# Performance work log

Measured on AMD Instinct MI355X. Metric: run time of the kernel, lower is better.

Reference implementation:

```python
import jax, jax.numpy as jnp
import numpy as np

BN_EPS = 1e-5


def setup_inputs() -> dict:
    key = jax.random.key(0)
    ks = jax.random.split(key, 6)
    B, C, N = 8, 256, 4096
    C4 = C // 4
    return {
        "x": jax.random.normal(ks[0], (B, C, N), dtype=jnp.float32),
        "w_qk": jax.random.normal(ks[1], (C4, C), dtype=jnp.float32) * 0.05,  # shared q/k weight
        "w_v": jax.random.normal(ks[2], (C, C), dtype=jnp.float32) * 0.05,
        "b_v": jax.random.normal(ks[3], (C,), dtype=jnp.float32) * 0.05,
        "w_t": jax.random.normal(ks[4], (C, C), dtype=jnp.float32) * 0.05,
        "b_t": jax.random.normal(ks[5], (C,), dtype=jnp.float32) * 0.05,
        "gamma": jnp.ones((C,), dtype=jnp.float32),
        "beta": jnp.zeros((C,), dtype=jnp.float32),
        "run_mean": jnp.zeros((C,), dtype=jnp.float32),
        "run_var": jnp.ones((C,), dtype=jnp.float32),
    }


def reference(x, w_qk, w_v, b_v, w_t, b_t, gamma, beta, run_mean, run_var):
    # x: [B, C, N]; 1x1 Conv1d == channel matmul.
    x_q = jnp.einsum('oc,bcn->bno', w_qk, x)               # [B, N, C/4]
    x_k = jnp.einsum('oc,bcn->bon', w_qk, x)               # [B, C/4, N]
    energy = jnp.einsum('bno,bom->bnm', x_q, x_k)          # [B, N, N], NO 1/sqrt(d) scaling
    attn = jax.nn.softmax(energy, axis=-1)                 # softmax over last dim only
    x_v = jnp.einsum('oc,bcn->bon', w_v, x) + b_v[None, :, None]  # [B, C, N]
    x_r = jnp.einsum('bcn,bnm->bcm', x_v, attn)            # V @ attn (right-multiply, no transpose)
    t = jnp.einsum('oc,bcn->bon', w_t, x - x_r) + b_t[None, :, None]
    # BatchNorm1d (inference): per-channel affine with running stats
    inv = gamma / jnp.sqrt(run_var + BN_EPS)
    bn = t * inv[None, :, None] + (beta - run_mean * inv)[None, :, None]
    return x + jnp.maximum(bn, 0.0)
```

## Files before the change

kernel.cpp:

```cpp
#include <hip/hip_runtime.h>

#define Bb 8
#define Cc 256
#define C4 64
#define Nn 4096

typedef _Float16 half8 __attribute__((ext_vector_type(8)));
typedef float f32x4 __attribute__((ext_vector_type(4)));
typedef unsigned int u32;

__device__ __forceinline__ f32x4 fz4() {
  f32x4 z; z[0] = 0.f; z[1] = 0.f; z[2] = 0.f; z[3] = 0.f; return z;
}
__device__ __forceinline__ f32x4 mfma16(half8 a, half8 b, f32x4 c) {
  return __builtin_amdgcn_mfma_f32_16x16x32_f16(a, b, c, 0, 0, 0);
}
__device__ __forceinline__ u32 pkrtz(float a, float b) {
  typedef __fp16 h2n __attribute__((ext_vector_type(2)));
  h2n h = __builtin_amdgcn_cvt_pkrtz(a, b);
  return __builtin_bit_cast(u32, h);
}
__device__ __forceinline__ void gll16(const void* g, void* l) {
  __builtin_amdgcn_global_load_lds(
      (const __attribute__((address_space(1))) u32*)g,
      (__attribute__((address_space(3))) u32*)l, 16, 0, 0);
}


__global__ void k0_weights(const float* __restrict__ wqk, const float* __restrict__ wv,
                           const float* __restrict__ wt,
                           _Float16* __restrict__ wqkh, _Float16* __restrict__ wqkl,
                           _Float16* __restrict__ wvf, _Float16* __restrict__ wtf) {
  int idx = blockIdx.x * 256 + threadIdx.x;
  if (idx < C4 * Cc) {
    int o = idx >> 8, c = idx & 255;
    float f = wqk[idx] * 1.2011224087864498f;
    _Float16 h = (_Float16)f;
    int off = ((((o >> 4) * 8 + (c >> 5)) * 4 + ((c >> 3) & 3)) * 16 + (o & 15)) * 8 + (c & 7);
    wqkh[off] = h;
    wqkl[off] = (_Float16)(f - (float)h);
  }
  if (idx < Cc * Cc) {
    int o = idx >> 8, k = idx & 255;
    int off = ((((o >> 4) * 8 + (k >> 5)) * 4 + ((k >> 3) & 3)) * 16 + (o & 15)) * 8 + (k & 7);
    wvf[off] = (_Float16)wv[idx];
    wtf[off] = (_Float16)wt[idx];
  }
}

__global__ __launch_bounds__(512) void k23_qkv(
    const float* __restrict__ x,
    const _Float16* __restrict__ wqkh, const _Float16* __restrict__ wqkl,
    const _Float16* __restrict__ wvf, const float* __restrict__ bv,
    _Float16* __restrict__ qkf, _Float16* __restrict__ xvf) {
  __shared__ _Float16 xh[64 * 264];
  const int bid = blockIdx.x;
  const int b = bid & 7, n0 = (bid >> 3) * 64, tid = threadIdx.x;
  {
    const int cc = tid >> 3, nn = (tid & 7) * 8;
    #pragma unroll
    for (int ph = 0; ph < 4; ++ph) {
      int c = cc + ph * 64;
      const float* src = x + ((size_t)(b * Cc + c)) * Nn + n0 + nn;
      float4 v0 = *(const float4*)(src);
      float4 v1 = *(const float4*)(src + 4);
      float vv[8] = {v0.x, v0.y, v0.z, v0.w, v1.x, v1.y, v1.z, v1.w};
      #pragma unroll
      for (int j = 0; j < 8; ++j) xh[(nn + j) * 264 + c] = (_Float16)vv[j];
    }
  }
  __syncthreads();
  const int w = tid >> 6, lane = tid & 63, l15 = lane & 15, l4 = lane >> 4;
  {
    const int fn = w >> 1, ob = (w & 1) * 32;
    f32x4 acc[2] = {fz4(), fz4()};
    #pragma unroll
    for (int kb = 0; kb < 8; ++kb) {
      half8 ah = *(const half8*)(xh + (fn * 16 + l15) * 264 + kb * 32 + l4 * 8);
      #pragma unroll
      for (int f = 0; f < 2; ++f) {
        const int ot = (ob >> 4) + f;
        half8 bh = *(const half8*)((const char*)wqkh + (ot * 8 + kb) * 1024 + lane * 16);
        half8 bl = *(const half8*)((const char*)wqkl + (ot * 8 + kb) * 1024 + lane * 16);
        acc[f] = mfma16(ah, bh, acc[f]);
        acc[f] = mfma16(ah, bl, acc[f]);
      }
    }
    #pragma unroll
    for (int f = 0; f < 2; ++f)
      #pragma unroll
      for (int i = 0; i < 4; ++i) {
        const int n = n0 + fn * 16 + l4 * 4 + i;
        const int o = ob + f * 16 + l15;
        int off = ((((b * 256 + (n >> 4)) * 2 + (o >> 5)) * 4 + ((o >> 3) & 3)) * 16 +
                   (n & 15)) * 8 + (o & 7);
        qkf[off] = (_Float16)acc[f][i];
      }
  }
  {
    const int cb = w * 32;
    f32x4 acc[2][4];
    #pragma unroll
    for (int a = 0; a < 2; ++a)
      #pragma unroll
      for (int q = 0; q < 4; ++q) acc[a][q] = fz4();
    #pragma unroll
    for (int kb = 0; kb < 8; ++kb) {
      half8 bfr[4];
      #pragma unroll
      for (int fnb = 0; fnb < 4; ++fnb)
        bfr[fnb] = *(const half8*)(xh + (fnb * 16 + l15) * 264 + kb * 32 + l4 * 8);
      #pragma unroll
      for (int fc = 0; fc < 2; ++fc) {
        const int ct = (cb >> 4) + fc;
        half8 a = *(const half8*)((const char*)wvf + (ct * 8 + kb) * 1024 + lane * 16);
        #pragma unroll
        for (int fnb = 0; fnb < 4; ++fnb)
          acc[fc][fnb] = mfma16(a, bfr[fnb], acc[fc][fnb]);
      }
    }
    #pragma unroll
    for (int fc = 0; fc < 2; ++fc)
      #pragma unroll
      for (int fnb = 0; fnb < 4; ++fnb)
        #pragma unroll
        for (int i = 0; i < 4; ++i) {
          const int c = cb + fc * 16 + l4 * 4 + i;
          const int n = n0 + fnb * 16 + l15;
          int off = ((((b * 16 + (c >> 4)) * 128 + (n >> 5)) * 4 + ((n >> 3) & 3)) * 16 +
                     (c & 15)) * 8 + (n & 7);
          xvf[off] = (_Float16)(acc[fc][fnb][i] + bv[c]);
        }
  }
}

__global__ __launch_bounds__(512, 4) void k4_stats(
    const _Float16* __restrict__ qkf, float* __restrict__ stats) {
  __shared__ float red[64][8];
  const int bid = blockIdx.x;
  const int b = bid & 7, n0 = (bid >> 3) * 64, tid = threadIdx.x;
  const int w = tid >> 6, lane = tid & 63, l15 = lane & 15, l4 = lane >> 4;
  const char* qbt = (const char*)qkf + (size_t)b * 524288;

  half8 qn_r[2][4];
  #pragma unroll
  for (int kb = 0; kb < 2; ++kb)
    #pragma unroll
    for (int fn = 0; fn < 4; ++fn)
      qn_r[kb][fn] = *(const half8*)(qbt + (((n0 >> 4) + fn) * 2 + kb) * 1024 + lane * 16);

  const char* qp = qbt + w * 2048 + lane * 16;
  half8 qa0 = *(const half8*)qp;
  half8 qa1 = *(const half8*)(qp + 1024);

  float sm[4] = {0.f, 0.f, 0.f, 0.f};
  for (int it = 0; it < 32; ++it) {
    f32x4 g[4] = {fz4(), fz4(), fz4(), fz4()};
    #pragma unroll
    for (int fn = 0; fn < 4; ++fn) g[fn] = mfma16(qa0, qn_r[0][fn], g[fn]);
    #pragma unroll
    for (int fn = 0; fn < 4; ++fn) g[fn] = mfma16(qa1, qn_r[1][fn], g[fn]);
    if (it < 31) qp += 16384;
    qa0 = *(const half8*)qp;
    qa1 = *(const half8*)(qp + 1024);
    #pragma unroll
    for (int fn = 0; fn < 4; ++fn)
      #pragma unroll
      for (int i = 0; i < 4; ++i)
        sm[fn] += exp2f(g[fn][i] - 32.0f);
  }
  #pragma unroll
  for (int fn = 0; fn < 4; ++fn) {
    sm[fn] += __shfl_xor(sm[fn], 16, 64);
    sm[fn] += __shfl_xor(sm[fn], 32, 64);
  }
  if (l4 == 0) {
    #pragma unroll
    for (int fn = 0; fn < 4; ++fn) red[fn * 16 + l15][w] = sm[fn];
  }
  __syncthreads();
  if (tid < 64) {
    float t = 0.f;
    #pragma unroll
    for (int j = 0; j < 8; ++j) t += red[tid][j];
    stats[(size_t)b * Nn + n0 + tid] = 32.0f + log2f(t);
  }
}

__global__ __launch_bounds__(512, 4) void k5_main(
    const float* __restrict__ x,
    const _Float16* __restrict__ qkf, const _Float16* __restrict__ xvf,
    const float* __restrict__ stats,
    const _Float16* __restrict__ wtf, const float* __restrict__ bt,
    const float* __restrict__ gamma, const float* __restrict__ beta,
    const float* __restrict__ rmean, const float* __restrict__ rvar,
    float* __restrict__ out) {
  __shared__ __align__(16) char smem[73728];
  const int bid = blockIdx.x;
  const int b = bid & 7, m0 = (bid >> 3) * 64, tid = threadIdx.x;
  const int w = tid >> 6, lane = tid & 63, l15 = lane & 15, l4 = lane >> 4;
  const int wa = w >> 2;
  const int wb = w & 3;
  const size_t bq = (size_t)b * Nn;
  const char* qkt = (const char*)qkf + (size_t)b * 524288;
  const char* xvt = (const char*)xvf + (size_t)b * 2097152;
  const int key = l15 & 7;
  char* xvw = smem + 40960 + (w << 12);

  half8 qm_r[2][2];
  #pragma unroll
  for (int kb = 0; kb < 2; ++kb)
    #pragma unroll
    for (int fm = 0; fm < 2; ++fm)
      qm_r[kb][fm] = *(const half8*)(qkt + (((m0 >> 4) + wa * 2 + fm) * 2 + kb) * 1024 +
                                     lane * 16);

  const char* qnsrc = qkt + 16384 + (size_t)tid * 16;
  const char* xvsrc[4];
  #pragma unroll
  for (int j = 0; j < 4; ++j)
    xvsrc[j] = xvt + ((w * 2 + (j >> 1)) * 128 + (j & 1)) * 1024 + (size_t)lane * 16;
  const float* anp = stats + bq + wb * 16 + l4 * 4;

  f32x4 acc[4][2];
  #pragma unroll
  for (int a = 0; a < 4; ++a)
    #pragma unroll
    for (int q = 0; q < 2; ++q) acc[a][q] = fz4();

  gll16(qkt + (size_t)tid * 16, smem + w * 1024);
  gll16(qkt + 8192 + (size_t)tid * 16, smem + 8192 + w * 1024);
  #pragma unroll
  for (int j = 0; j < 4; ++j) gll16(xvsrc[j], xvw + j * 1024);
  float4 an = *(const float4*)anp;
  asm volatile("s_waitcnt vmcnt(0) lgkmcnt(0)" ::: "memory");
  __builtin_amdgcn_sched_barrier(0);
  __builtin_amdgcn_s_barrier();

  int br = 0, bw = 2;
  for (int it = 0; it < 64; ++it) {
    gll16(qnsrc, smem + bw * 8192 + w * 1024);
    if (it < 61) qnsrc += 8192;
    bw = bw == 2 ? 0 : bw + 1;
    const char* qb = smem + br * 8192;
    br = br == 2 ? 0 : br + 1;
    f32x4 g0 = fz4(), g1 = fz4();
    #pragma unroll
    for (int kb = 0; kb < 2; ++kb) {
      half8 ah = *(const half8*)(qb + wb * 2048 + kb * 1024 + lane * 16);
      g0 = mfma16(ah, qm_r[kb][0], g0);
      g1 = mfma16(ah, qm_r[kb][1], g1);
    }
    char* PTp = smem + 24576 + ((it & 1) << 13);
    {
      uint2 pk;
      pk.x = pkrtz(exp2f(g0[0] - an.x), exp2f(g0[1] - an.y));
      pk.y = pkrtz(exp2f(g0[2] - an.z), exp2f(g0[3] - an.w));
      *(uint2*)(PTp + (wa * 32 + l15) * 128 + ((wb * 32 + l4 * 8) ^ (key << 4))) = pk;
      pk.x = pkrtz(exp2f(g1[0] - an.x), exp2f(g1[1] - an.y));
      pk.y = pkrtz(exp2f(g1[2] - an.z), exp2f(g1[3] - an.w));
      *(uint2*)(PTp + (wa * 32 + 16 + l15) * 128 + ((wb * 32 + l4 * 8) ^ (key << 4))) = pk;
    }
    if (it < 63) anp += 64;
    an = *(const float4*)anp;
    asm volatile("s_waitcnt vmcnt(2) lgkmcnt(0)" ::: "memory");
    __builtin_amdgcn_sched_barrier(0);
    __builtin_amdgcn_s_barrier();
    __builtin_amdgcn_s_setprio(1);
    #pragma unroll
    for (int kb = 0; kb < 2; ++kb) {
      half8 pa[4], xb[2];
      #pragma unroll
      for (int fm = 0; fm < 4; ++fm)
        pa[fm] = *(const half8*)(PTp + (fm * 16 + l15) * 128 + (((kb * 4 + l4) ^ key) * 16));
      #pragma unroll
      for (int fc = 0; fc < 2; ++fc)
        xb[fc] = *(const half8*)(xvw + (fc * 2 + kb) * 1024 + lane * 16);
      #pragma unroll
      for (int fm = 0; fm < 4; ++fm)
        #pragma unroll
        for (int fc = 0; fc < 2; ++fc)
          acc[fm][fc] = mfma16(pa[fm], xb[fc], acc[fm][fc]);
    }
    __builtin_amdgcn_s_setprio(0);
    asm volatile("s_waitcnt lgkmcnt(0)" ::: "memory");
    __builtin_amdgcn_sched_barrier(0);
    if (it < 63) {
      #pragma unroll
      for (int j = 0; j < 4; ++j) xvsrc[j] += 2048;
    }
    #pragma unroll
    for (int j = 0; j < 4; ++j) gll16(xvsrc[j], xvw + j * 1024);
  }
  asm volatile("s_waitcnt vmcnt(0) lgkmcnt(0)" ::: "memory");
  __builtin_amdgcn_sched_barrier(0);
  __builtin_amdgcn_s_barrier();

  _Float16* st = (_Float16*)smem;
  #pragma unroll
  for (int fm = 0; fm < 4; ++fm)
    #pragma unroll
    for (int fc = 0; fc < 2; ++fc) {
      int c = w * 32 + fc * 16 + l15;
      const float* xp = x + ((size_t)b * Cc + c) * Nn + m0 + fm * 16 + l4 * 4;
      float4 v = *(const float4*)xp;
      float vv[4] = {v.x, v.y, v.z, v.w};
      #pragma unroll
      for (int i = 0; i < 4; ++i) {
        int m = fm * 16 + l4 * 4 + i;
        st[m * 264 + c] = (_Float16)(vv[i] - acc[fm][fc][i]);
      }
    }
  __syncthreads();
  {
    const int ob = (w >> 1) * 64, mb2 = (w & 1) * 32;
    f32x4 t[4][2];
    #pragma unroll
    for (int a = 0; a < 4; ++a)
      #pragma unroll
      for (int q = 0; q < 2; ++q) t[a][q] = fz4();
    #pragma unroll
    for (int kb = 0; kb < 8; ++kb) {
      half8 bfr[2];
      #pragma unroll
      for (int fm2 = 0; fm2 < 2; ++fm2)
        bfr[fm2] = *(const half8*)(st + (mb2 + fm2 * 16 + l15) * 264 + kb * 32 + l4 * 8);
      #pragma unroll
      for (int fo = 0; fo < 4; ++fo) {
        const int ot = (ob >> 4) + fo;
        half8 a = *(const half8*)((const char*)wtf + (ot * 8 + kb) * 1024 + lane * 16);
        #pragma unroll
        for (int fm2 = 0; fm2 < 2; ++fm2)
          t[fo][fm2] = mfma16(a, bfr[fm2], t[fo][fm2]);
      }
    }
    #pragma unroll
    for (int fo = 0; fo < 4; ++fo)
      #pragma unroll
      for (int i = 0; i < 4; ++i) {
        const int o = ob + fo * 16 + l4 * 4 + i;
        const float inv = gamma[o] * rsqrtf(rvar[o] + 1e-5f);
        const float addv = beta[o] - rmean[o] * inv;
        const float btv = bt[o];
        #pragma unroll
        for (int fm2 = 0; fm2 < 2; ++fm2) {
          const int m = m0 + mb2 + fm2 * 16 + l15;
          float tv = t[fo][fm2][i] + btv;
          float bn = tv * inv + addv;
          float xr = x[((size_t)b * Cc + o) * Nn + m];
          out[((size_t)b * Cc + o) * Nn + m] = xr + fmaxf(bn, 0.0f);
        }
      }
  }
}

extern "C" void kernel_launch(void* const* d_in, const int* in_sizes, int n_in,
                              void* d_out, int out_size, void* d_ws, size_t ws_size,
                              hipStream_t stream) {
  const float* x = (const float*)d_in[0];
  const float* wqk = (const float*)d_in[1];
  const float* wv = (const float*)d_in[2];
  const float* bv = (const float*)d_in[3];
  const float* wt = (const float*)d_in[4];
  const float* bt = (const float*)d_in[5];
  const float* gamma = (const float*)d_in[6];
  const float* beta = (const float*)d_in[7];
  const float* rmean = (const float*)d_in[8];
  const float* rvar = (const float*)d_in[9];
  float* out = (float*)d_out;

  char* ws = (char*)d_ws;
  size_t off = 0;
  auto alloc = [&](size_t nb) {
    char* p = ws + off;
    off += (nb + 255) & ~(size_t)255;
    return p;
  };
  _Float16* qkf = (_Float16*)alloc((size_t)Bb * Nn * C4 * 2);
  _Float16* xvf = (_Float16*)alloc((size_t)Bb * Cc * Nn * 2);
  float* stats = (float*)alloc((size_t)Bb * Nn * 4);
  _Float16* wqkh = (_Float16*)alloc((size_t)C4 * Cc * 2);
  _Float16* wqkl = (_Float16*)alloc((size_t)C4 * Cc * 2);
  _Float16* wvf = (_Float16*)alloc((size_t)Cc * Cc * 2);
  _Float16* wtf = (_Float16*)alloc((size_t)Cc * Cc * 2);

  k0_weights<<<dim3(256), dim3(256), 0, stream>>>(wqk, wv, wt, wqkh, wqkl, wvf, wtf);
  k23_qkv<<<dim3(512), dim3(512), 0, stream>>>(x, wqkh, wqkl, wvf, bv, qkf, xvf);
  k4_stats<<<dim3(512), dim3(512), 0, stream>>>(qkf, stats);
  k5_main<<<dim3(512), dim3(512), 0, stream>>>(x, qkf, xvf, stats, wtf, bt,
                                               gamma, beta, rmean, rvar, out);
}
```

Baseline: 164.9 us.

## Double output tile per block in attention kernel and use raw v_exp_f32

The main attention kernel now handles 128 output columns per block instead of 64. Its 8 waves are laid out as a 2x4 grid, each computing a 64x64 accumulator tile, and the xv tiles are double-buffered in a shared LDS region. This halves the grid to 256 blocks and doubles reuse of each streamed V tile and each softmax probability tile. The cost is more LDS (120KB) and more registers, with launch bounds lowered to 2 blocks per CU. exp2f is also replaced with a raw v_exp_f32 instruction to avoid range-handling overhead, at the risk of losing denormal or edge-case accuracy.

```diff
diff --git a/kernel.cpp b/kernel.cpp
--- a/kernel.cpp
+++ b/kernel.cpp
@@ -19,6 +19,11 @@
   typedef __fp16 h2n __attribute__((ext_vector_type(2)));
   h2n h = __builtin_amdgcn_cvt_pkrtz(a, b);
   return __builtin_bit_cast(u32, h);
+}
+__device__ __forceinline__ float ex2(float x) {
+  float r;
+  asm("v_exp_f32 %0, %1" : "=v"(r) : "v"(x));
+  return r;
 }
 __device__ __forceinline__ void gll16(const void* g, void* l) {
   __builtin_amdgcn_global_load_lds(
@@ -167,7 +172,7 @@
     for (int fn = 0; fn < 4; ++fn)
       #pragma unroll
       for (int i = 0; i < 4; ++i)
-        sm[fn] += exp2f(g[fn][i] - 32.0f);
+        sm[fn] += ex2(g[fn][i] - 32.0f);
   }
   #pragma unroll
   for (int fn = 0; fn < 4; ++fn) {
@@ -187,7 +192,7 @@
   }
 }
 
-__global__ __launch_bounds__(512, 4) void k5_main(
+__global__ __launch_bounds__(512, 2) void k5_main(
     const float* __restrict__ x,
     const _Float16* __restrict__ qkf, const _Float16* __restrict__ xvf,
     const float* __restrict__ stats,
@@ -195,9 +200,9 @@
     const float* __restrict__ gamma, const float* __restrict__ beta,
     const float* __restrict__ rmean, const float* __restrict__ rvar,
     float* __restrict__ out) {
-  __shared__ __align__(16) char smem[73728];
+  __shared__ __align__(16) char smem[122880];
   const int bid = blockIdx.x;
-  const int b = bid & 7, m0 = (bid >> 3) * 64, tid = threadIdx.x;
+  const int b = bid & 7, m0 = (bid >> 3) * 128, tid = threadIdx.x;
   const int w = tid >> 6, lane = tid & 63, l15 = lane & 15, l4 = lane >> 4;
   const int wa = w >> 2;
   const int wb = w & 3;
@@ -205,33 +210,30 @@
   const char* qkt = (const char*)qkf + (size_t)b * 524288;
   const char* xvt = (const char*)xvf + (size_t)b * 2097152;
   const int key = l15 & 7;
-  char* xvw = smem + 40960 + (w << 12);
-
-  half8 qm_r[2][2];
+
+  half8 qm_r[2][4];
   #pragma unroll
   for (int kb = 0; kb < 2; ++kb)
     #pragma unroll
-    for (int fm = 0; fm < 2; ++fm)
-      qm_r[kb][fm] = *(const half8*)(qkt + (((m0 >> 4) + wa * 2 + fm) * 2 + kb) * 1024 +
+    for (int fm = 0; fm < 4; ++fm)
+      qm_r[kb][fm] = *(const half8*)(qkt + ((((m0 >> 4) + wa * 4 + fm) * 2) + kb) * 1024 +
                                      lane * 16);
 
   const char* qnsrc = qkt + 16384 + (size_t)tid * 16;
-  const char* xvsrc[4];
-  #pragma unroll
-  for (int j = 0; j < 4; ++j)
-    xvsrc[j] = xvt + ((w * 2 + (j >> 1)) * 128 + (j & 1)) * 1024 + (size_t)lane * 16;
+  const char* xvp = xvt + (size_t)w * 262144 + (size_t)lane * 16;
   const float* anp = stats + bq + wb * 16 + l4 * 4;
 
-  f32x4 acc[4][2];
+  f32x4 acc[4][4];
   #pragma unroll
   for (int a = 0; a < 4; ++a)
     #pragma unroll
-    for (int q = 0; q < 2; ++q) acc[a][q] = fz4();
+    for (int q = 0; q < 4; ++q) acc[a][q] = fz4();
 
   gll16(qkt + (size_t)tid * 16, smem + w * 1024);
   gll16(qkt + 8192 + (size_t)tid * 16, smem + 8192 + w * 1024);
   #pragma unroll
-  for (int j = 0; j < 4; ++j) gll16(xvsrc[j], xvw + j * 1024);
+  for (int j = 0; j < 4; ++j)
+    gll16(xvp + (j >> 1) * 131072 + (j & 1) * 1024, smem + 57344 + (w * 4 + j) * 1024);
   float4 an = *(const float4*)anp;
   asm volatile("s_waitcnt vmcnt(0) lgkmcnt(0)" ::: "memory");
   __builtin_amdgcn_sched_barrier(0);
@@ -244,53 +246,52 @@
     bw = bw == 2 ? 0 : bw + 1;
     const char* qb = smem + br * 8192;
     br = br == 2 ? 0 : br + 1;
-    f32x4 g0 = fz4(), g1 = fz4();
+    f32x4 g[4] = {fz4(), fz4(), fz4(), fz4()};
     #pragma unroll
     for (int kb = 0; kb < 2; ++kb) {
-      half8 ah = *(const half8*)(qb + wb * 2048 + kb * 1024 + lane * 16);
-      g0 = mfma16(ah, qm_r[kb][0], g0);
-      g1 = mfma16(ah, qm_r[kb][1], g1);
-    }
-    char* PTp = smem + 24576 + ((it & 1) << 13);
-    {
+      half8 ah = *(const half8*)(qb + (wb * 2 + kb) * 1024 + lane * 16);
+      #pragma unroll
+      for (int fm = 0; fm < 4; ++fm)
+        g[fm] = mfma16(ah, qm_r[kb][fm], g[fm]);
+    }
+    char* PTp = smem + 24576 + ((it & 1) << 14);
+    #pragma unroll
+    for (int fm = 0; fm < 4; ++fm) {
       uint2 pk;
-      pk.x = pkrtz(exp2f(g0[0] - an.x), exp2f(g0[1] - an.y));
-      pk.y = pkrtz(exp2f(g0[2] - an.z), exp2f(g0[3] - an.w));
-      *(uint2*)(PTp + (wa * 32 + l15) * 128 + ((wb * 32 + l4 * 8) ^ (key << 4))) = pk;
-      pk.x = pkrtz(exp2f(g1[0] - an.x), exp2f(g1[1] - an.y));
-      pk.y = pkrtz(exp2f(g1[2] - an.z), exp2f(g1[3] - an.w));
-      *(uint2*)(PTp + (wa * 32 + 16 + l15) * 128 + ((wb * 32 + l4 * 8) ^ (key << 4))) = pk;
+      pk.x = pkrtz(ex2(g[fm][0] - an.x), ex2(g[fm][1] - an.y));
+      pk.y = pkrtz(ex2(g[fm][2] - an.z), ex2(g[fm][3] - an.w));
+      *(uint2*)(PTp + (wa * 64 + fm * 16 + l15) * 128 +
+                ((wb * 32 + l4 * 8) ^ (key << 4))) = pk;
     }
     if (it < 63) anp += 64;
     an = *(const float4*)anp;
     asm volatile("s_waitcnt vmcnt(2) lgkmcnt(0)" ::: "memory");
     __builtin_amdgcn_sched_barrier(0);
     __builtin_amdgcn_s_barrier();
+    const char* xvR = smem + 57344 + ((it & 1) << 15);
     __builtin_amdgcn_s_setprio(1);
     #pragma unroll
     for (int kb = 0; kb < 2; ++kb) {
-      half8 pa[4], xb[2];
+      half8 pa[4], xb[4];
       #pragma unroll
       for (int fm = 0; fm < 4; ++fm)
-        pa[fm] = *(const half8*)(PTp + (fm * 16 + l15) * 128 + (((kb * 4 + l4) ^ key) * 16));
-      #pragma unroll
-      for (int fc = 0; fc < 2; ++fc)
-        xb[fc] = *(const half8*)(xvw + (fc * 2 + kb) * 1024 + lane * 16);
+        pa[fm] = *(const half8*)(PTp + (wa * 64 + fm * 16 + l15) * 128 +
+                                 (((kb * 4 + l4) ^ key) * 16));
+      #pragma unroll
+      for (int fc = 0; fc < 4; ++fc)
+        xb[fc] = *(const half8*)(xvR + ((wb * 4 + fc) * 2 + kb) * 1024 + lane * 16);
       #pragma unroll
       for (int fm = 0; fm < 4; ++fm)
         #pragma unroll
-        for (int fc = 0; fc < 2; ++fc)
+        for (int fc = 0; fc < 4; ++fc)
           acc[fm][fc] = mfma16(pa[fm], xb[fc], acc[fm][fc]);
     }
     __builtin_amdgcn_s_setprio(0);
-    asm volatile("s_waitcnt lgkmcnt(0)" ::: "memory");
-    __builtin_amdgcn_sched_barrier(0);
-    if (it < 63) {
-      #pragma unroll
-      for (int j = 0; j < 4; ++j) xvsrc[j] += 2048;
-    }
-    #pragma unroll
-    for (int j = 0; j < 4; ++j) gll16(xvsrc[j], xvw + j * 1024);
+    if (it < 63) xvp += 2048;
+    char* xvD = smem + 57344 + (((it + 1) & 1) << 15) + (w * 4) * 1024;
+    #pragma unroll
+    for (int j = 0; j < 4; ++j)
+      gll16(xvp + (j >> 1) * 131072 + (j & 1) * 1024, xvD + j * 1024);
   }
   asm volatile("s_waitcnt vmcnt(0) lgkmcnt(0)" ::: "memory");
   __builtin_amdgcn_sched_barrier(0);
@@ -300,37 +301,36 @@
   #pragma unroll
   for (int fm = 0; fm < 4; ++fm)
     #pragma unroll
-    for (int fc = 0; fc < 2; ++fc) {
-      int c = w * 32 + fc * 16 + l15;
-      const float* xp = x + ((size_t)b * Cc + c) * Nn + m0 + fm * 16 + l4 * 4;
+    for (int fc = 0; fc < 4; ++fc) {
+      int c = wb * 64 + fc * 16 + l15;
+      int mb = wa * 64 + fm * 16 + l4 * 4;
+      const float* xp = x + ((size_t)b * Cc + c) * Nn + m0 + mb;
       float4 v = *(const float4*)xp;
       float vv[4] = {v.x, v.y, v.z, v.w};
       #pragma unroll
-      for (int i = 0; i < 4; ++i) {
-        int m = fm * 16 + l4 * 4 + i;
-        st[m * 264 + c] = (_Float16)(vv[i] - acc[fm][fc][i]);
-      }
+      for (int i = 0; i < 4; ++i)
+        st[(mb + i) * 264 + c] = (_Float16)(vv[i] - acc[fm][fc][i]);
     }
   __syncthreads();
   {
-    const int ob = (w >> 1) * 64, mb2 = (w & 1) * 32;
-    f32x4 t[4][2];
+    const int ob = wb * 64, mh = wa * 64;
+    f32x4 t[4][4];
     #pragma unroll
     for (int a = 0; a < 4; ++a)
       #pragma unroll
-      for (int q = 0; q < 2; ++q) t[a][q] = fz4();
+      for (int q = 0; q < 4; ++q) t[a][q] = fz4();
     #pragma unroll
     for (int kb = 0; kb < 8; ++kb) {
-      half8 bfr[2];
-      #pragma unroll
-      for (int fm2 = 0; fm2 < 2; ++fm2)
-        bfr[fm2] = *(const half8*)(st + (mb2 + fm2 * 16 + l15) * 264 + kb * 32 + l4 * 8);
+      half8 bfr[4];
+      #pragma unroll
+      for (int fm2 = 0; fm2 < 4; ++fm2)
+        bfr[fm2] = *(const half8*)(st + (mh + fm2 * 16 + l15) * 264 + kb * 32 + l4 * 8);
       #pragma unroll
       for (int fo = 0; fo < 4; ++fo) {
         const int ot = (ob >> 4) + fo;
         half8 a = *(const half8*)((const char*)wtf + (ot * 8 + kb) * 1024 + lane * 16);
         #pragma unroll
-        for (int fm2 = 0; fm2 < 2; ++fm2)
+        for (int fm2 = 0; fm2 < 4; ++fm2)
           t[fo][fm2] = mfma16(a, bfr[fm2], t[fo][fm2]);
       }
     }
@@ -343,8 +343,8 @@
         const float addv = beta[o] - rmean[o] * inv;
         const float btv = bt[o];
         #pragma unroll
-        for (int fm2 = 0; fm2 < 2; ++fm2) {
-          const int m = m0 + mb2 + fm2 * 16 + l15;
+        for (int fm2 = 0; fm2 < 4; ++fm2) {
+          const int m = m0 + mh + fm2 * 16 + l15;
           float tv = t[fo][fm2][i] + btv;
           float bn = tv * inv + addv;
           float xr = x[((size_t)b * Cc + o) * Nn + m];
@@ -387,6 +387,6 @@
   k0_weights<<<dim3(256), dim3(256), 0, stream>>>(wqk, wv, wt, wqkh, wqkl, wvf, wtf);
   k23_qkv<<<dim3(512), dim3(512), 0, stream>>>(x, wqkh, wqkl, wvf, bv, qkf, xvf);
   k4_stats<<<dim3(512), dim3(512), 0, stream>>>(qkf, stats);
-  k5_main<<<dim3(512), dim3(512), 0, stream>>>(x, qkf, xvf, stats, wtf, bt,
+  k5_main<<<dim3(256), dim3(512), 0, stream>>>(x, qkf, xvf, stats, wtf, bt,
                                                gamma, beta, rmean, rvar, out);
 }
```

After: 149.2 us. 9.5% less time.
